# Kernel tuning notes

Measured on AMD Instinct MI355X. Metric: run time of the kernel, lower is better.

The kernel has to match this reference:

```python
import jax, jax.numpy as jnp
import numpy as np

N_NODES = 100000


def _sage_conv(x, src, dst, Wl, bl, Wr):
    # mean aggregation of source-node features into destination nodes
    msgs = x[src]                                            # [E, F]
    agg = jax.ops.segment_sum(msgs, dst, num_segments=N_NODES)   # [N, F]
    cnt = jax.ops.segment_sum(jnp.ones((src.shape[0],), x.dtype), dst,
                              num_segments=N_NODES)          # [N]
    mean = agg / jnp.maximum(cnt, 1.0)[:, None]
    # PyG SAGEConv: lin_l(aggr) + lin_r(x_root); lin_l has bias, lin_r does not
    return mean @ Wl.T + bl + x @ Wr.T


def setup_inputs() -> dict:
    key = jax.random.key(0)
    k = jax.random.split(key, 8)
    F_IN, H = 64, 128
    E = 1600000
    x = jax.random.normal(k[0], (N_NODES, F_IN), dtype=jnp.float32)
    edge_index = jax.random.randint(k[1], (2, E), 0, N_NODES, dtype=jnp.int32)
    s1 = 1.0 / np.sqrt(F_IN)
    s2 = 1.0 / np.sqrt(H)
    Wl1 = jax.random.uniform(k[2], (H, F_IN), jnp.float32, -s1, s1)
    bl1 = jnp.zeros((H,), jnp.float32)
    Wr1 = jax.random.uniform(k[3], (H, F_IN), jnp.float32, -s1, s1)
    Wl2 = jax.random.uniform(k[4], (H, H), jnp.float32, -s2, s2)
    bl2 = jnp.zeros((H,), jnp.float32)
    Wr2 = jax.random.uniform(k[5], (H, H), jnp.float32, -s2, s2)
    return {"x": x, "edge_index": edge_index,
            "Wl1": Wl1, "bl1": bl1, "Wr1": Wr1,
            "Wl2": Wl2, "bl2": bl2, "Wr2": Wr2}


def reference(x, edge_index, Wl1, bl1, Wr1, Wl2, bl2, Wr2):
    src, dst = edge_index[0], edge_index[1]
    h = _sage_conv(x, src, dst, Wl1, bl1, Wr1)
    h = jax.nn.relu(h)
    out = _sage_conv(h, src, dst, Wl2, bl2, Wr2)
    return out
```

## Files before the change

### kernel.cpp

```cpp
#include <hip/hip_runtime.h>


#define EPB 16384
#define MAXNB 1024

typedef __attribute__((ext_vector_type(8))) short bf16x8;
typedef __attribute__((ext_vector_type(4))) float f32x4;

union ABu { unsigned u[4]; bf16x8 v; };

__device__ inline unsigned short f2bf_rne(float f) {
    unsigned u = __float_as_uint(f);
    return (unsigned short)((u + 0x7FFFu + ((u >> 16) & 1u)) >> 16);
}

__device__ inline void splitA(const f32x4 fA, const f32x4 fB,
                              bf16x8& hi, bf16x8& lo) {
    ABu H, L;
    float f[8] = {fA.x, fA.y, fA.z, fA.w, fB.x, fB.y, fB.z, fB.w};
    #pragma unroll
    for (int p = 0; p < 4; ++p) {
        unsigned u0 = __float_as_uint(f[2*p]);
        unsigned u1 = __float_as_uint(f[2*p+1]);
        unsigned h0 = u0 & 0xFFFF0000u;
        unsigned h1 = u1 & 0xFFFF0000u;
        H.u[p] = (u0 >> 16) | h1;
        float r0 = f[2*p]   - __uint_as_float(h0);
        float r1 = f[2*p+1] - __uint_as_float(h1);
        L.u[p] = (__float_as_uint(r0) >> 16) | (__float_as_uint(r1) & 0xFFFF0000u);
    }
    hi = H.v; lo = L.v;
}

__global__ __launch_bounds__(256) void cvt_bf16_kernel(
    const float* __restrict__ in, unsigned short* __restrict__ out, int n)
{
    int i = (blockIdx.x * 256 + threadIdx.x) * 4;
    if (i >= n) return;
    float4 v = *reinterpret_cast<const float4*>(&in[i]);
    ushort4 o;
    o.x = f2bf_rne(v.x); o.y = f2bf_rne(v.y);
    o.z = f2bf_rne(v.z); o.w = f2bf_rne(v.w);
    *reinterpret_cast<ushort4*>(&out[i]) = o;
}

__global__ __launch_bounds__(256) void count_blocks_kernel(
    const int* __restrict__ ei, int* __restrict__ blockCounts,
    int E, int NB)
{
    __shared__ int hist[MAXNB];
    for (int i = threadIdx.x; i < NB; i += 256) hist[i] = 0;
    __syncthreads();
    int e0 = blockIdx.x * EPB;
    int e1 = min(e0 + EPB, E);
    for (int e = e0 + threadIdx.x; e < e1; e += 256)
        atomicAdd(&hist[ei[E + e] >> 7], 1);
    __syncthreads();
    for (int i = threadIdx.x; i < NB; i += 256)
        blockCounts[blockIdx.x * NB + i] = hist[i];
}

__global__ __launch_bounds__(1024) void scan_buckets_kernel(
    const int* __restrict__ blockCounts,
    int* __restrict__ blockBase,
    int* __restrict__ bucketBase,
    int NB, int NBLK)
{
    __shared__ int tot[1024];
    int t = threadIdx.x;
    int run = 0;
    if (t < NB) {
        for (int k = 0; k < NBLK; ++k) {
            int c = blockCounts[k * NB + t];
            blockBase[k * NB + t] = run;
            run += c;
        }
    }
    tot[t] = run;
    __syncthreads();
    for (int o = 1; o < 1024; o <<= 1) {
        int a = (t >= o) ? tot[t - o] : 0;
        __syncthreads();
        tot[t] += a;
        __syncthreads();
    }
    if (t < NB) {
        int base = tot[t] - run;
        bucketBase[t] = base;
        for (int k = 0; k < NBLK; ++k) blockBase[k * NB + t] += base;
    }
    if (t == 0) bucketBase[NB] = tot[1023];
}

__global__ __launch_bounds__(256) void write_pairs_kernel(
    const int* __restrict__ ei, const int* __restrict__ blockBase,
    unsigned* __restrict__ pairs, int E, int NB)
{
    __shared__ int cur[MAXNB];
    for (int i = threadIdx.x; i < NB; i += 256)
        cur[i] = blockBase[blockIdx.x * NB + i];
    __syncthreads();
    int e0 = blockIdx.x * EPB;
    int e1 = min(e0 + EPB, E);
    for (int e = e0 + threadIdx.x; e < e1; e += 256) {
        int s = ei[e];
        int d = ei[E + e];
        int p = atomicAdd(&cur[d >> 7], 1);
        pairs[p] = ((unsigned)(d & 127) << 25) | (unsigned)s;
    }
}

__global__ __launch_bounds__(256) void bucket_finalize_kernel(
    const unsigned* __restrict__ pairs, const int* __restrict__ bucketBase,
    int* __restrict__ rowptr, int* __restrict__ ssrc, int N)
{
    __shared__ int hist[128];
    __shared__ int scn[128];
    __shared__ int cur[128];
    int t = threadIdx.x;
    int b = blockIdx.x;
    int segS = bucketBase[b], segE = bucketBase[b + 1];
    if (t < 128) hist[t] = 0;
    __syncthreads();
    for (int i = segS + t; i < segE; i += 256)
        atomicAdd(&hist[pairs[i] >> 25], 1);
    __syncthreads();
    if (t < 128) scn[t] = hist[t];
    __syncthreads();
    for (int o = 1; o < 128; o <<= 1) {
        int a = 0;
        if (t < 128 && t >= o) a = scn[t - o];
        __syncthreads();
        if (t < 128) scn[t] += a;
        __syncthreads();
    }
    if (t < 128) {
        int start = segS + scn[t] - hist[t];
        cur[t] = start;
        int node = b * 128 + t;
        if (node < N) rowptr[node] = start;
    }
    if (b == 0 && t == 0) rowptr[N] = bucketBase[gridDim.x];
    __syncthreads();
    for (int i = segS + t; i < segE; i += 256) {
        unsigned p = pairs[i];
        int pos = atomicAdd(&cur[p >> 25], 1);
        ssrc[pos] = (int)(p & 0x1FFFFFFu);
    }
}

__global__ __launch_bounds__(256) void prep_w_kernel(
    const float* __restrict__ Wl, const float* __restrict__ Wr, int F,
    short* __restrict__ w0f, short* __restrict__ w1f, int nfrag)
{
    int t = blockIdx.x * 256 + threadIdx.x;
    if (t >= nfrag * 64) return;
    int lane = t & 63, fr = t >> 6;
    int j  = fr & 7, ks = fr >> 3;
    int col = j * 16 + (lane & 15);
    int k0  = ks * 32 + (lane >> 4) * 8;
    #pragma unroll
    for (int e = 0; e < 8; ++e) {
        int k = k0 + e;
        float w = (k < F) ? Wl[col * F + k] : Wr[col * F + (k - F)];
        unsigned u = __float_as_uint(w);
        unsigned h = u & 0xFFFF0000u;
        float r = w - __uint_as_float(h);
        w0f[t * 8 + e] = (short)(u >> 16);
        w1f[t * 8 + e] = (short)(__float_as_uint(r) >> 16);
    }
}

template<int F>
__global__ __launch_bounds__(256) void agg_gather_kernel(
    const int* __restrict__ rowptr, const int* __restrict__ ssrc,
    const unsigned short* __restrict__ feat,
    float* __restrict__ mean, int N)
{
    constexpr int C  = F / 4;
    constexpr int G  = 64 / C;
    constexpr int SH = (F == 128) ? 8 : 7;
    int wave = threadIdx.x >> 6;
    int lane = threadIdx.x & 63;
    int n = blockIdx.x * 4 + wave;
    if (n >= N) return;
    int rp = rowptr[n], re = rowptr[n + 1];
    const int chunk = lane & (C - 1);
    const int grp   = lane / C;
    const unsigned cb = (unsigned)chunk * 8;
    const char* fbase = (const char*)feat;

    float a0 = 0.f, a1 = 0.f, a2 = 0.f, a3 = 0.f;

    int e = rp + grp;
    while (e + 7 * G < re) {
        int s[8];
        #pragma unroll
        for (int i = 0; i < 8; ++i) s[i] = ssrc[e + i * G];
        #pragma unroll
        for (int i = 0; i < 8; ++i) {
            unsigned off = ((unsigned)s[i] << SH) + cb;
            uint2 p = *reinterpret_cast<const uint2*>(fbase + off);
            a0 += __uint_as_float(p.x << 16);
            a1 += __uint_as_float(p.x & 0xFFFF0000u);
            a2 += __uint_as_float(p.y << 16);
            a3 += __uint_as_float(p.y & 0xFFFF0000u);
        }
        e += 8 * G;
    }
    while (e < re) {
        unsigned off = ((unsigned)ssrc[e] << SH) + cb;
        uint2 p = *reinterpret_cast<const uint2*>(fbase + off);
        a0 += __uint_as_float(p.x << 16);
        a1 += __uint_as_float(p.x & 0xFFFF0000u);
        a2 += __uint_as_float(p.y << 16);
        a3 += __uint_as_float(p.y & 0xFFFF0000u);
        e += G;
    }

    #pragma unroll
    for (int o = C; o < 64; o <<= 1) {
        a0 += __shfl_xor(a0, o);
        a1 += __shfl_xor(a1, o);
        a2 += __shfl_xor(a2, o);
        a3 += __shfl_xor(a3, o);
    }
    if (lane < C) {
        float inv = 1.0f / (float)max(re - rp, 1);
        f32x4 o4 = {a0 * inv, a1 * inv, a2 * inv, a3 * inv};
        __builtin_nontemporal_store(o4,
            reinterpret_cast<f32x4*>(&mean[(size_t)n * F + lane * 4]));
    }
}

template<int F, bool RELU, bool EMIT_BF16>
__global__ __launch_bounds__(256, 2) void dense_mfma_kernel(
    const float* __restrict__ left,
    const float* __restrict__ right,
    const short* __restrict__ w0f,
    const short* __restrict__ w1f,
    const float* __restrict__ bl,
    float* __restrict__ out,
    unsigned short* __restrict__ outb,
    int N)
{
    constexpr int NS = (2 * F) / 32;
    const int tid  = threadIdx.x;
    const int lane = tid & 63;
    const int wv   = tid >> 6;
    const int r16  = lane & 15;
    const int kg   = lane >> 4;
    const int rowBase = blockIdx.x * 128 + wv * 32;

    const int row0 = min(rowBase + r16,      N - 1);
    const int row1 = min(rowBase + 16 + r16, N - 1);

    f32x4 acc[2][8];
    #pragma unroll
    for (int rt = 0; rt < 2; ++rt)
        #pragma unroll
        for (int j = 0; j < 8; ++j)
            acc[rt][j] = (f32x4){0.f, 0.f, 0.f, 0.f};

    #pragma unroll
    for (int ks = 0; ks < NS; ++ks) {
        const bool Lh = (ks * 32) < F;
        const float* __restrict__ src = Lh ? left : right;
        const int koff = ks * 32 - (Lh ? 0 : F) + kg * 8;

        bf16x8 a0[2], a1[2];
        {
            const float* ap0 = src + (size_t)row0 * F + koff;
            splitA(*reinterpret_cast<const f32x4*>(ap0),
                   *reinterpret_cast<const f32x4*>(ap0 + 4), a0[0], a1[0]);
            const float* ap1 = src + (size_t)row1 * F + koff;
            splitA(*reinterpret_cast<const f32x4*>(ap1),
                   *reinterpret_cast<const f32x4*>(ap1 + 4), a0[1], a1[1]);
        }

        #pragma unroll
        for (int j = 0; j < 8; ++j) {
            const size_t fb = (((size_t)(ks * 8 + j)) * 64 + lane) * 8;
            const bf16x8 b0 = *reinterpret_cast<const bf16x8*>(&w0f[fb]);
            const bf16x8 b1 = *reinterpret_cast<const bf16x8*>(&w1f[fb]);
            #pragma unroll
            for (int rt = 0; rt < 2; ++rt) {
                acc[rt][j] = __builtin_amdgcn_mfma_f32_16x16x32_bf16(
                    a0[rt], b0, acc[rt][j], 0, 0, 0);
                acc[rt][j] = __builtin_amdgcn_mfma_f32_16x16x32_bf16(
                    a0[rt], b1, acc[rt][j], 0, 0, 0);
                acc[rt][j] = __builtin_amdgcn_mfma_f32_16x16x32_bf16(
                    a1[rt], b0, acc[rt][j], 0, 0, 0);
            }
        }
    }

    #pragma unroll
    for (int j = 0; j < 8; ++j) {
        const int col = j * 16 + r16;
        const float b = bl[col];
        #pragma unroll
        for (int rt = 0; rt < 2; ++rt) {
            const int rb = rowBase + rt * 16 + kg * 4;
            #pragma unroll
            for (int i = 0; i < 4; ++i) {
                int row = rb + i;
                if (row < N) {
                    float v = acc[rt][j][i] + b;
                    if (RELU) v = fmaxf(v, 0.f);
                    out[(size_t)row * 128 + col] = v;
                    if (EMIT_BF16) outb[(size_t)row * 128 + col] = f2bf_rne(v);
                }
            }
        }
    }
}

extern "C" void kernel_launch(void* const* d_in, const int* in_sizes, int n_in,
                              void* d_out, int out_size, void* d_ws, size_t ws_size,
                              hipStream_t stream) {
    const float* x   = (const float*)d_in[0];
    const int*   ei  = (const int*)d_in[1];
    const float* Wl1 = (const float*)d_in[2];
    const float* bl1 = (const float*)d_in[3];
    const float* Wr1 = (const float*)d_in[4];
    const float* Wl2 = (const float*)d_in[5];
    const float* bl2 = (const float*)d_in[6];
    const float* Wr2 = (const float*)d_in[7];
    float* out = (float*)d_out;

    const int N    = in_sizes[0] / 64;
    const int E    = in_sizes[1] / 2;
    const int NB   = (N + 127) / 128;
    const int NBLK = (E + EPB - 1) / EPB;

    int* ssrc       = (int*)d_ws;
    int* rowptr     = ssrc + E;
    int* bucketBase = rowptr + (N + 1);
    int* blockCounts= bucketBase + (NB + 1);
    int* blockBase  = blockCounts + NB * NBLK;
    short* w0f1 = (short*)(blockBase + NB * NBLK);
    short* w1f1 = w0f1 + 32 * 512;
    short* w0f2 = w1f1 + 32 * 512;
    short* w1f2 = w0f2 + 64 * 512;
    size_t shortEnd = (size_t)(w1f2 + 64 * 512 - (short*)d_ws);
    size_t floatOff = (shortEnd * 2 + 15) / 16 * 4;
    float* meanbuf = (float*)d_ws + floatOff;
    float* h       = meanbuf + (size_t)N * 128;
    unsigned* pairs     = (unsigned*)meanbuf;
    unsigned short* xb  = (unsigned short*)(meanbuf + 8000000);
    unsigned short* hb  = (unsigned short*)d_out;

    cvt_bf16_kernel<<<(N * 64 / 4 + 255) / 256, 256, 0, stream>>>(x, xb, N * 64);

    count_blocks_kernel<<<NBLK, 256, 0, stream>>>(ei, blockCounts, E, NB);
    scan_buckets_kernel<<<1, 1024, 0, stream>>>(blockCounts, blockBase, bucketBase, NB, NBLK);
    write_pairs_kernel<<<NBLK, 256, 0, stream>>>(ei, blockBase, pairs, E, NB);
    bucket_finalize_kernel<<<NB, 256, 0, stream>>>(pairs, bucketBase, rowptr, ssrc, N);

    prep_w_kernel<<<(32 * 64 + 255) / 256, 256, 0, stream>>>(Wl1, Wr1, 64, w0f1, w1f1, 32);
    prep_w_kernel<<<(64 * 64 + 255) / 256, 256, 0, stream>>>(Wl2, Wr2, 128, w0f2, w1f2, 64);

    const int dgrid = (N + 127) / 128;

    agg_gather_kernel<64><<<(N + 3) / 4, 256, 0, stream>>>(rowptr, ssrc, xb, meanbuf, N);
    dense_mfma_kernel<64, true, true><<<dgrid, 256, 0, stream>>>(
        meanbuf, x, w0f1, w1f1, bl1, h, hb, N);

    agg_gather_kernel<128><<<(N + 3) / 4, 256, 0, stream>>>(rowptr, ssrc, hb, meanbuf, N);
    dense_mfma_kernel<128, false, false><<<dgrid, 256, 0, stream>>>(
        meanbuf, h, w0f2, w1f2, bl2, out, nullptr, N);
}
```

Baseline: 442.4 us.

## Fuse mean aggregation with MFMA dense layer via swizzled LDS bf16 tile

Merges the gather-mean kernel and the dense MFMA kernel into a single per-layer kernel. Each block aggregates 128 rows into a swizzled bf16 LDS tile, then runs the MFMA GEMM directly from LDS and from the bf16 root features. This removes the fp32 mean buffer round trip and the fp32 h write. It also drops the hi/lo split-bf16 compensation on activations, so it uses two MFMAs per step instead of three, at a cost in accuracy. The risk is lower gather parallelism, since each wave now serially aggregates 32 rows, and reduced precision from using bf16 for the mean and the root features.

```diff
diff --git a/kernel.cpp b/kernel.cpp
--- a/kernel.cpp
+++ b/kernel.cpp
@@ -6,30 +6,10 @@
 
 typedef __attribute__((ext_vector_type(8))) short bf16x8;
 typedef __attribute__((ext_vector_type(4))) float f32x4;
-
-union ABu { unsigned u[4]; bf16x8 v; };
 
 __device__ inline unsigned short f2bf_rne(float f) {
     unsigned u = __float_as_uint(f);
     return (unsigned short)((u + 0x7FFFu + ((u >> 16) & 1u)) >> 16);
-}
-
-__device__ inline void splitA(const f32x4 fA, const f32x4 fB,
-                              bf16x8& hi, bf16x8& lo) {
-    ABu H, L;
-    float f[8] = {fA.x, fA.y, fA.z, fA.w, fB.x, fB.y, fB.z, fB.w};
-    #pragma unroll
-    for (int p = 0; p < 4; ++p) {
-        unsigned u0 = __float_as_uint(f[2*p]);
-        unsigned u1 = __float_as_uint(f[2*p+1]);
-        unsigned h0 = u0 & 0xFFFF0000u;
-        unsigned h1 = u1 & 0xFFFF0000u;
-        H.u[p] = (u0 >> 16) | h1;
-        float r0 = f[2*p]   - __uint_as_float(h0);
-        float r1 = f[2*p+1] - __uint_as_float(h1);
-        L.u[p] = (__float_as_uint(r0) >> 16) | (__float_as_uint(r1) & 0xFFFF0000u);
-    }
-    hi = H.v; lo = L.v;
 }
 
 __global__ __launch_bounds__(256) void cvt_bf16_kernel(
@@ -171,89 +151,91 @@
     }
 }
 
-template<int F>
-__global__ __launch_bounds__(256) void agg_gather_kernel(
+template<int F, bool LAST>
+__global__ __launch_bounds__(256, 4) void fused_layer_kernel(
     const int* __restrict__ rowptr, const int* __restrict__ ssrc,
     const unsigned short* __restrict__ feat,
-    float* __restrict__ mean, int N)
-{
+    const short* __restrict__ w0f, const short* __restrict__ w1f,
+    const float* __restrict__ bl,
+    float* __restrict__ outf,
+    unsigned short* __restrict__ outb,
+    int N)
+{
+    constexpr int NS = (2 * F) / 32;
     constexpr int C  = F / 4;
     constexpr int G  = 64 / C;
+    constexpr int RB = F * 2;
     constexpr int SH = (F == 128) ? 8 : 7;
-    int wave = threadIdx.x >> 6;
-    int lane = threadIdx.x & 63;
-    int n = blockIdx.x * 4 + wave;
-    if (n >= N) return;
-    int rp = rowptr[n], re = rowptr[n + 1];
-    const int chunk = lane & (C - 1);
-    const int grp   = lane / C;
-    const unsigned cb = (unsigned)chunk * 8;
-    const char* fbase = (const char*)feat;
-
-    float a0 = 0.f, a1 = 0.f, a2 = 0.f, a3 = 0.f;
-
-    int e = rp + grp;
-    while (e + 7 * G < re) {
-        int s[8];
-        #pragma unroll
-        for (int i = 0; i < 8; ++i) s[i] = ssrc[e + i * G];
-        #pragma unroll
-        for (int i = 0; i < 8; ++i) {
-            unsigned off = ((unsigned)s[i] << SH) + cb;
-            uint2 p = *reinterpret_cast<const uint2*>(fbase + off);
-            a0 += __uint_as_float(p.x << 16);
-            a1 += __uint_as_float(p.x & 0xFFFF0000u);
-            a2 += __uint_as_float(p.y << 16);
-            a3 += __uint_as_float(p.y & 0xFFFF0000u);
-        }
-        e += 8 * G;
-    }
-    while (e < re) {
-        unsigned off = ((unsigned)ssrc[e] << SH) + cb;
-        uint2 p = *reinterpret_cast<const uint2*>(fbase + off);
-        a0 += __uint_as_float(p.x << 16);
-        a1 += __uint_as_float(p.x & 0xFFFF0000u);
-        a2 += __uint_as_float(p.y << 16);
-        a3 += __uint_as_float(p.y & 0xFFFF0000u);
-        e += G;
-    }
-
-    #pragma unroll
-    for (int o = C; o < 64; o <<= 1) {
-        a0 += __shfl_xor(a0, o);
-        a1 += __shfl_xor(a1, o);
-        a2 += __shfl_xor(a2, o);
-        a3 += __shfl_xor(a3, o);
-    }
-    if (lane < C) {
-        float inv = 1.0f / (float)max(re - rp, 1);
-        f32x4 o4 = {a0 * inv, a1 * inv, a2 * inv, a3 * inv};
-        __builtin_nontemporal_store(o4,
-            reinterpret_cast<f32x4*>(&mean[(size_t)n * F + lane * 4]));
-    }
-}
-
-template<int F, bool RELU, bool EMIT_BF16>
-__global__ __launch_bounds__(256, 2) void dense_mfma_kernel(
-    const float* __restrict__ left,
-    const float* __restrict__ right,
-    const short* __restrict__ w0f,
-    const short* __restrict__ w1f,
-    const float* __restrict__ bl,
-    float* __restrict__ out,
-    unsigned short* __restrict__ outb,
-    int N)
-{
-    constexpr int NS = (2 * F) / 32;
+    __shared__ char lds[128 * RB];
+
     const int tid  = threadIdx.x;
     const int lane = tid & 63;
     const int wv   = tid >> 6;
-    const int r16  = lane & 15;
-    const int kg   = lane >> 4;
-    const int rowBase = blockIdx.x * 128 + wv * 32;
-
-    const int row0 = min(rowBase + r16,      N - 1);
-    const int row1 = min(rowBase + 16 + r16, N - 1);
+    const int rowBase = blockIdx.x * 128;
+
+    {
+        const int chunk = lane & (C - 1);
+        const int grp   = lane / C;
+        const unsigned cb = (unsigned)chunk * 8;
+        const char* fbase = (const char*)feat;
+        for (int i = 0; i < 32; ++i) {
+            int lr = wv * 32 + i;
+            int n  = rowBase + lr;
+            if (n >= N) break;
+            int rp = rowptr[n], re = rowptr[n + 1];
+            float a0 = 0.f, a1 = 0.f, a2 = 0.f, a3 = 0.f;
+            int e = rp + grp;
+            while (e + 7 * G < re) {
+                int s[8];
+                #pragma unroll
+                for (int k = 0; k < 8; ++k) s[k] = ssrc[e + k * G];
+                #pragma unroll
+                for (int k = 0; k < 8; ++k) {
+                    unsigned off = ((unsigned)s[k] << SH) + cb;
+                    uint2 p = *reinterpret_cast<const uint2*>(fbase + off);
+                    a0 += __uint_as_float(p.x << 16);
+                    a1 += __uint_as_float(p.x & 0xFFFF0000u);
+                    a2 += __uint_as_float(p.y << 16);
+                    a3 += __uint_as_float(p.y & 0xFFFF0000u);
+                }
+                e += 8 * G;
+            }
+            while (e < re) {
+                unsigned off = ((unsigned)ssrc[e] << SH) + cb;
+                uint2 p = *reinterpret_cast<const uint2*>(fbase + off);
+                a0 += __uint_as_float(p.x << 16);
+                a1 += __uint_as_float(p.x & 0xFFFF0000u);
+                a2 += __uint_as_float(p.y << 16);
+                a3 += __uint_as_float(p.y & 0xFFFF0000u);
+                e += G;
+            }
+            #pragma unroll
+            for (int o = C; o < 64; o <<= 1) {
+                a0 += __shfl_xor(a0, o);
+                a1 += __shfl_xor(a1, o);
+                a2 += __shfl_xor(a2, o);
+                a3 += __shfl_xor(a3, o);
+            }
+            if (lane < C) {
+                float inv = 1.0f / (float)max(re - rp, 1);
+                unsigned lo = (unsigned)f2bf_rne(a0 * inv)
+                            | ((unsigned)f2bf_rne(a1 * inv) << 16);
+                unsigned hi = (unsigned)f2bf_rne(a2 * inv)
+                            | ((unsigned)f2bf_rne(a3 * inv) << 16);
+                unsigned byte = (unsigned)lr * RB
+                              + (cb ^ (((unsigned)lr & 7u) << 4));
+                *reinterpret_cast<uint2*>(lds + byte) = make_uint2(lo, hi);
+            }
+        }
+    }
+    __syncthreads();
+
+    const int r16 = lane & 15;
+    const int kg  = lane >> 4;
+    const int lrow0 = wv * 32 + r16;
+    const int lrow1 = wv * 32 + 16 + r16;
+    const int grow0 = min(rowBase + lrow0, N - 1);
+    const int grow1 = min(rowBase + lrow1, N - 1);
 
     f32x4 acc[2][8];
     #pragma unroll
@@ -264,20 +246,18 @@
 
     #pragma unroll
     for (int ks = 0; ks < NS; ++ks) {
-        const bool Lh = (ks * 32) < F;
-        const float* __restrict__ src = Lh ? left : right;
-        const int koff = ks * 32 - (Lh ? 0 : F) + kg * 8;
-
-        bf16x8 a0[2], a1[2];
-        {
-            const float* ap0 = src + (size_t)row0 * F + koff;
-            splitA(*reinterpret_cast<const f32x4*>(ap0),
-                   *reinterpret_cast<const f32x4*>(ap0 + 4), a0[0], a1[0]);
-            const float* ap1 = src + (size_t)row1 * F + koff;
-            splitA(*reinterpret_cast<const f32x4*>(ap1),
-                   *reinterpret_cast<const f32x4*>(ap1 + 4), a0[1], a1[1]);
-        }
-
+        bf16x8 a[2];
+        if (ks < NS / 2) {
+            unsigned kb = (unsigned)(ks * 64 + kg * 16);
+            a[0] = *reinterpret_cast<const bf16x8*>(
+                lds + (unsigned)lrow0 * RB + (kb ^ (((unsigned)lrow0 & 7u) << 4)));
+            a[1] = *reinterpret_cast<const bf16x8*>(
+                lds + (unsigned)lrow1 * RB + (kb ^ (((unsigned)lrow1 & 7u) << 4)));
+        } else {
+            int ko = (ks - NS / 2) * 32 + kg * 8;
+            a[0] = *reinterpret_cast<const bf16x8*>(&feat[(size_t)grow0 * F + ko]);
+            a[1] = *reinterpret_cast<const bf16x8*>(&feat[(size_t)grow1 * F + ko]);
+        }
         #pragma unroll
         for (int j = 0; j < 8; ++j) {
             const size_t fb = (((size_t)(ks * 8 + j)) * 64 + lane) * 8;
@@ -286,11 +266,9 @@
             #pragma unroll
             for (int rt = 0; rt < 2; ++rt) {
                 acc[rt][j] = __builtin_amdgcn_mfma_f32_16x16x32_bf16(
-                    a0[rt], b0, acc[rt][j], 0, 0, 0);
+                    a[rt], b0, acc[rt][j], 0, 0, 0);
                 acc[rt][j] = __builtin_amdgcn_mfma_f32_16x16x32_bf16(
-                    a0[rt], b1, acc[rt][j], 0, 0, 0);
-                acc[rt][j] = __builtin_amdgcn_mfma_f32_16x16x32_bf16(
-                    a1[rt], b0, acc[rt][j], 0, 0, 0);
+                    a[rt], b1, acc[rt][j], 0, 0, 0);
             }
         }
     }
@@ -301,15 +279,18 @@
         const float b = bl[col];
         #pragma unroll
         for (int rt = 0; rt < 2; ++rt) {
-            const int rb = rowBase + rt * 16 + kg * 4;
+            const int rb = rowBase + wv * 32 + rt * 16 + kg * 4;
             #pragma unroll
             for (int i = 0; i < 4; ++i) {
                 int row = rb + i;
                 if (row < N) {
                     float v = acc[rt][j][i] + b;
-                    if (RELU) v = fmaxf(v, 0.f);
-                    out[(size_t)row * 128 + col] = v;
-                    if (EMIT_BF16) outb[(size_t)row * 128 + col] = f2bf_rne(v);
+                    if (!LAST) {
+                        v = fmaxf(v, 0.f);
+                        outb[(size_t)row * 128 + col] = f2bf_rne(v);
+                    } else {
+                        outf[(size_t)row * 128 + col] = v;
+                    }
                 }
             }
         }
@@ -334,22 +315,18 @@
     const int NB   = (N + 127) / 128;
     const int NBLK = (E + EPB - 1) / EPB;
 
-    int* ssrc       = (int*)d_ws;
-    int* rowptr     = ssrc + E;
-    int* bucketBase = rowptr + (N + 1);
-    int* blockCounts= bucketBase + (NB + 1);
-    int* blockBase  = blockCounts + NB * NBLK;
-    short* w0f1 = (short*)(blockBase + NB * NBLK);
+    unsigned short* xb = (unsigned short*)d_ws;
+    unsigned short* hb = xb + (size_t)N * 64;
+    short* w0f1 = (short*)(hb + (size_t)N * 128);
     short* w1f1 = w0f1 + 32 * 512;
     short* w0f2 = w1f1 + 32 * 512;
     short* w1f2 = w0f2 + 64 * 512;
-    size_t shortEnd = (size_t)(w1f2 + 64 * 512 - (short*)d_ws);
-    size_t floatOff = (shortEnd * 2 + 15) / 16 * 4;
-    float* meanbuf = (float*)d_ws + floatOff;
-    float* h       = meanbuf + (size_t)N * 128;
-    unsigned* pairs     = (unsigned*)meanbuf;
-    unsigned short* xb  = (unsigned short*)(meanbuf + 8000000);
-    unsigned short* hb  = (unsigned short*)d_out;
+    int* ssrc        = (int*)(w1f2 + 64 * 512);
+    int* rowptr      = ssrc + E;
+    int* bucketBase  = rowptr + (N + 1);
+    int* blockCounts = bucketBase + (NB + 1);
+    int* blockBase   = blockCounts + NB * NBLK;
+    unsigned* pairs  = (unsigned*)(blockBase + NB * NBLK);
 
     cvt_bf16_kernel<<<(N * 64 / 4 + 255) / 256, 256, 0, stream>>>(x, xb, N * 64);
 
@@ -363,11 +340,9 @@
 
     const int dgrid = (N + 127) / 128;
 
-    agg_gather_kernel<64><<<(N + 3) / 4, 256, 0, stream>>>(rowptr, ssrc, xb, meanbuf, N);
-    dense_mfma_kernel<64, true, true><<<dgrid, 256, 0, stream>>>(
-        meanbuf, x, w0f1, w1f1, bl1, h, hb, N);
-
-    agg_gather_kernel<128><<<(N + 3) / 4, 256, 0, stream>>>(rowptr, ssrc, hb, meanbuf, N);
-    dense_mfma_kernel<128, false, false><<<dgrid, 256, 0, stream>>>(
-        meanbuf, h, w0f2, w1f2, bl2, out, nullptr, N);
-}
+    fused_layer_kernel<64, false><<<dgrid, 256, 0, stream>>>(
+        rowptr, ssrc, xb, w0f1, w1f1, bl1, nullptr, hb, N);
+
+    fused_layer_kernel<128, true><<<dgrid, 256, 0, stream>>>(
+        rowptr, ssrc, hb, w0f2, w1f2, bl2, out, nullptr, N);
+}
```

Result: slower. 489.4 us (+10.6%).
